# Kernel tuning notes

Hardware: AMD Instinct MI355X
Metric: run time of the kernel (lower is better)

## Reference

```python
import jax, jax.numpy as jnp
import numpy as np


def setup_inputs() -> dict:
    key = jax.random.key(0)
    k1, k2, k3, k4, k5, k6 = jax.random.split(key, 6)
    Ne, dim_in, dim_out, B, Nr, E = 100000, 128, 128, 4, 8, 200000
    return {
        "H": jax.random.normal(k1, (Ne, dim_in), dtype=jnp.float32),
        "A": jax.random.uniform(k2, (Nr, B), dtype=jnp.float32),
        "V": jax.random.uniform(k3, (B, dim_in, dim_out), dtype=jnp.float32),
        "edge_row": jax.random.randint(k4, (Nr, E), 0, Ne, dtype=jnp.int32),
        "edge_col": jax.random.randint(k5, (Nr, E), 0, Ne, dtype=jnp.int32),
        "edge_val": jax.random.uniform(k6, (Nr, E), dtype=jnp.float32),
    }


def reference(H, A, V, edge_row, edge_col, edge_val):
    # W = einsum('rb,bio->rio', A, V): basis-decomposed relation weights
    Ne = H.shape[0]
    Nr = A.shape[0]
    W = jnp.einsum('rb,bio->rio', A, V)            # [Nr, dim_in, dim_out]
    HxW = jnp.einsum('ni,rio->rno', H, W)          # [Nr, Ne, dim_out]
    # sparse T_r @ HxW_r: gather source rows (cols of T), scale by values,
    # scatter-add into destination rows. Done for all relations at once.
    msgs = HxW[jnp.arange(Nr)[:, None], edge_col] * edge_val[..., None]  # [Nr, E, dim_out]
    out = jax.ops.segment_sum(
        msgs.reshape(-1, msgs.shape[-1]),
        edge_row.reshape(-1),
        num_segments=Ne,
    )  # sum over relations folded into one segment_sum
    return out
```

## Files before the change

### kernel.cpp

```cpp
#include <hip/hip_runtime.h>

typedef __attribute__((ext_vector_type(8))) short short8;
typedef __attribute__((ext_vector_type(4))) float floatx4;
typedef __attribute__((ext_vector_type(2))) float floatx2;

constexpr int DIM   = 128;
constexpr int NB    = 4;
constexpr int NR    = 8;
constexpr int BROWS = 512;
constexpr int BCAP  = 16384;

static __device__ __forceinline__ unsigned short f2bf(float f) {
    unsigned int u = __float_as_uint(f);
    u += 0x7FFFu + ((u >> 16) & 1u);
    return (unsigned short)(u >> 16);
}
static __device__ __forceinline__ float bf_lo(unsigned int h) {
    return __uint_as_float(h << 16);
}
static __device__ __forceinline__ float bf_hi(unsigned int h) {
    return __uint_as_float(h & 0xFFFF0000u);
}

__global__ __launch_bounds__(256) void build_vfrag(
    const float* __restrict__ V, unsigned short* __restrict__ VfragG)
{
    int idx  = blockIdx.x * 256 + threadIdx.x;
    int lane = idx & 63;
    int ks   = (idx >> 6) & 3;
    int ot   = (idx >> 8) & 7;
    int b    = idx >> 11;

    int o  = ot * 16 + (lane & 15);
    int kb = ks * 32 + (lane >> 4) * 8;

    short8 v;
#pragma unroll
    for (int j = 0; j < 8; ++j)
        v[j] = (short)f2bf(V[((size_t)b * DIM + kb + j) * DIM + o]);
    *reinterpret_cast<short8*>(VfragG + (size_t)idx * 8) = v;
}

__global__ __launch_bounds__(256) void build_wfrag(
    const float* __restrict__ A, const float* __restrict__ V,
    unsigned short* __restrict__ Wfrag)
{
    int idx  = blockIdx.x * 256 + threadIdx.x;
    int lane = idx & 63;
    int ks   = (idx >> 6) & 3;
    int ot   = (idx >> 8) & 7;
    int r    = idx >> 11;

    int o     = ot * 16 + (lane & 15);
    int kbase = ks * 32 + (lane >> 4) * 8;

    float a0 = A[r * NB + 0], a1 = A[r * NB + 1];
    float a2 = A[r * NB + 2], a3 = A[r * NB + 3];

    short8 v;
#pragma unroll
    for (int j = 0; j < 8; ++j) {
        int k = kbase + j;
        float w = a0 * V[(0 * DIM + k) * DIM + o]
                + a1 * V[(1 * DIM + k) * DIM + o]
                + a2 * V[(2 * DIM + k) * DIM + o]
                + a3 * V[(3 * DIM + k) * DIM + o];
        v[j] = (short)f2bf(w);
    }
    *reinterpret_cast<short8*>(Wfrag + (size_t)idx * 8) = v;
}

__global__ __launch_bounds__(256) void h_to_bf(
    const float* __restrict__ H, unsigned short* __restrict__ Hbf, int n8)
{
    int i = blockIdx.x * 256 + threadIdx.x;
    if (i >= n8) return;
    const float4* hp = reinterpret_cast<const float4*>(H) + (size_t)i * 2;
    float4 f0 = hp[0];
    float4 f1 = hp[1];
    short8 v;
    v[0] = (short)f2bf(f0.x); v[1] = (short)f2bf(f0.y);
    v[2] = (short)f2bf(f0.z); v[3] = (short)f2bf(f0.w);
    v[4] = (short)f2bf(f1.x); v[5] = (short)f2bf(f1.y);
    v[6] = (short)f2bf(f1.z); v[7] = (short)f2bf(f1.w);
    *reinterpret_cast<short8*>(Hbf + (size_t)i * 8) = v;
}

__global__ __launch_bounds__(256) void bucket_scatter(
    const int* __restrict__ erow, const int* __restrict__ ecol,
    const float* __restrict__ eval, int* __restrict__ bcnt,
    int2* __restrict__ sorted1, int n, int E, int chunk)
{
    __shared__ int cnt[256];
    __shared__ int base[256];
    int t = threadIdx.x;
    cnt[t] = 0;
    __syncthreads();

    int s = blockIdx.x * chunk;
    int e = s + chunk; if (e > n) e = n;

    for (int i = s + t; i < e; i += 256)
        atomicAdd(&cnt[erow[i] >> 9], 1);
    __syncthreads();

    int c = cnt[t];
    base[t] = (c > 0) ? atomicAdd(&bcnt[t], c) : 0;
    cnt[t] = 0;
    __syncthreads();

    for (int i = s + t; i < e; i += 256) {
        int row = erow[i];
        int bkt = row >> 9;
        int rank = atomicAdd(&cnt[bkt], 1);
        int r = (int)((unsigned)i / (unsigned)E);
        int2 m;
        m.x = ((row & (BROWS - 1)) << 20) | (r << 17) | ecol[i];
        m.y = __float_as_int(eval[i]);
        sorted1[(size_t)bkt * BCAP + base[bkt] + rank] = m;
    }
}

__global__ __launch_bounds__(1024) void bucket_sort(
    const int2* __restrict__ sorted1, const int* __restrict__ bcnt,
    int* __restrict__ rowStart, int2* __restrict__ sorted, int Ne, int nbuc)
{
    __shared__ int hcnt[BROWS];
    __shared__ int hoff[BROWS];
    __shared__ int sd[256];
    int b = blockIdx.x;
    int t = threadIdx.x;

    for (int i = t; i < BROWS; i += 1024) hcnt[i] = 0;

    if (t < 256) sd[t] = (t < nbuc) ? bcnt[t] : 0;
    __syncthreads();
#pragma unroll
    for (int off = 1; off < 256; off <<= 1) {
        int v = (t < 256 && t >= off) ? sd[t - off] : 0;
        __syncthreads();
        if (t < 256) sd[t] += v;
        __syncthreads();
    }
    if (b == 0 && t == nbuc - 1) rowStart[Ne] = sd[t];

    int n  = bcnt[b];
    int bs = sd[b] - n;
    const int2* src = sorted1 + (size_t)b * BCAP;

    for (int i = t; i < n; i += 1024)
        atomicAdd(&hcnt[(unsigned)src[i].x >> 20], 1);
    __syncthreads();

    if (t < BROWS) hoff[t] = hcnt[t];
    __syncthreads();
#pragma unroll
    for (int off = 1; off < BROWS; off <<= 1) {
        int v = (t < BROWS && t >= off) ? hoff[t - off] : 0;
        __syncthreads();
        if (t < BROWS) hoff[t] += v;
        __syncthreads();
    }
    if (t < BROWS) hoff[t] -= hcnt[t];
    __syncthreads();

    int rs = b * BROWS;
    int nr = Ne - rs; if (nr > BROWS) nr = BROWS;
    for (int j = t; j < nr; j += 1024)
        rowStart[rs + j] = bs + hoff[j];

    for (int i = t; i < BROWS; i += 1024) hcnt[i] = 0;
    __syncthreads();

    for (int i = t; i < n; i += 1024) {
        int2 m = src[i];
        int lr = (unsigned)m.x >> 20;
        int pos = bs + hoff[lr] + atomicAdd(&hcnt[lr], 1);
        sorted[pos] = m;
    }
}

#define AGG_LOAD8(kk, vv, hh, base)                                          \
    _Pragma("unroll")                                                        \
    for (int u = 0; u < 8; ++u) {                                            \
        int2 m = sorted[(base) + u];                                         \
        kk[u] = __builtin_amdgcn_readfirstlane(m.x);                         \
        vv[u] = __uint_as_float(__builtin_amdgcn_readfirstlane(m.y));        \
    }                                                                        \
    _Pragma("unroll")                                                        \
    for (int u = 0; u < 8; ++u)                                              \
        hh[u] = reinterpret_cast<const unsigned int*>(                       \
            Hbf + (size_t)(kk[u] & 0x1FFFF) * DIM)[lane];

#define AGG_FMA8(kk, vv, hh)                                                 \
    _Pragma("unroll")                                                        \
    for (int u = 0; u < 8; ++u) {                                            \
        float4 a = Af[((unsigned)kk[u] >> 17) & 7];                          \
        floatx2 h; h[0] = bf_lo(hh[u]); h[1] = bf_hi(hh[u]);                 \
        float s0 = vv[u] * a.x, s1 = vv[u] * a.y;                            \
        float s2 = vv[u] * a.z, s3 = vv[u] * a.w;                            \
        acc[0] += (floatx2){s0, s0} * h;                                     \
        acc[1] += (floatx2){s1, s1} * h;                                     \
        acc[2] += (floatx2){s2, s2} * h;                                     \
        acc[3] += (floatx2){s3, s3} * h;                                     \
    }

__global__ __launch_bounds__(1024, 4) void fused_kernel(
    const unsigned short* __restrict__ Hbf,
    const int*  __restrict__ rowStart,
    const int2* __restrict__ sorted,
    const float* __restrict__ Aw,
    const unsigned short* __restrict__ VfragG,
    float* __restrict__ out, int Ne, int nTiles)
{
    __shared__ short8 ldsV[8192];
    __shared__ unsigned short ldsA[8192];

    int tid  = threadIdx.x;
    int wave = tid >> 6;
    int lane = tid & 63;
    int quad = lane >> 4, l15 = lane & 15;

    for (int i = tid; i < 8192; i += 1024)
        ldsV[i] = reinterpret_cast<const short8*>(VfragG)[i];

    const float4* Af = reinterpret_cast<const float4*>(Aw);

    unsigned short* aw = ldsA + (size_t)wave * 32
                       + (size_t)(lane >> 4) * 512
                       + (size_t)((lane >> 2) & 3) * 8
                       + (size_t)(lane & 3) * 2;

    for (int tile = blockIdx.x; tile < nTiles; tile += gridDim.x) {
        int node = tile * 16 + wave;
        floatx2 acc[4];
#pragma unroll
        for (int b = 0; b < 4; ++b) acc[b] = (floatx2){0.f, 0.f};

        if (node < Ne) {
            int s = __builtin_amdgcn_readfirstlane(rowStart[node]);
            int e = __builtin_amdgcn_readfirstlane(rowStart[node + 1]);
            int i = s;
            if (i + 8 <= e) {
                int kkA[8], kkB[8];
                float vvA[8], vvB[8];
                unsigned int hhA[8], hhB[8];
                AGG_LOAD8(kkA, vvA, hhA, i); i += 8;
                for (;;) {
                    if (i + 8 <= e) {
                        AGG_LOAD8(kkB, vvB, hhB, i); i += 8;
                        AGG_FMA8(kkA, vvA, hhA);
                    } else { AGG_FMA8(kkA, vvA, hhA); break; }
                    if (i + 8 <= e) {
                        AGG_LOAD8(kkA, vvA, hhA, i); i += 8;
                        AGG_FMA8(kkB, vvB, hhB);
                    } else { AGG_FMA8(kkB, vvB, hhB); break; }
                }
            }
            for (; i < e; ++i) {
                int2 m = sorted[i];
                int k = __builtin_amdgcn_readfirstlane(m.x);
                float v = __uint_as_float(__builtin_amdgcn_readfirstlane(m.y));
                unsigned int hu = reinterpret_cast<const unsigned int*>(
                    Hbf + (size_t)(k & 0x1FFFF) * DIM)[lane];
                float4 a = Af[((unsigned)k >> 17) & 7];
                floatx2 h; h[0] = bf_lo(hu); h[1] = bf_hi(hu);
                float s0 = v * a.x, s1 = v * a.y, s2 = v * a.z, s3 = v * a.w;
                acc[0] += (floatx2){s0, s0} * h;
                acc[1] += (floatx2){s1, s1} * h;
                acc[2] += (floatx2){s2, s2} * h;
                acc[3] += (floatx2){s3, s3} * h;
            }
        }
#pragma unroll
        for (int b = 0; b < 4; ++b) {
            unsigned int pk = (unsigned int)f2bf(acc[b][0])
                            | ((unsigned int)f2bf(acc[b][1]) << 16);
            *reinterpret_cast<unsigned int*>(aw + b * 2048) = pk;
        }
        __syncthreads();

        if (wave < 8) {
            int ot = wave;
            const short8* a8 = reinterpret_cast<const short8*>(ldsA);
            floatx4 vacc = (floatx4){0.f, 0.f, 0.f, 0.f};
#pragma unroll
            for (int b = 0; b < 4; ++b)
#pragma unroll
                for (int ks = 0; ks < 4; ++ks)
                    vacc = __builtin_amdgcn_mfma_f32_16x16x32_bf16(
                        ldsV[((b * 8 + ot) * 4 + ks) * 64 + lane],
                        a8[b * 256 + ks * 64 + l15 * 4 + quad],
                        vacc, 0, 0, 0);

            int onode = tile * 16 + l15;
            if (onode < Ne) {
                float4 st;
                st.x = vacc[0]; st.y = vacc[1]; st.z = vacc[2]; st.w = vacc[3];
                *reinterpret_cast<float4*>(
                    out + (size_t)onode * DIM + ot * 16 + quad * 4) = st;
            }
        }
        __syncthreads();
    }
}

__global__ __launch_bounds__(256) void rgcn_main(
    const unsigned short* __restrict__ Hbf,
    const unsigned short* __restrict__ Wfrag,
    const int*   __restrict__ erow,
    const int*   __restrict__ ecol,
    const float* __restrict__ eval,
    float*       __restrict__ out,
    int E, int groups_per_rel, int waves_per_rel)
{
    int wid  = blockIdx.x * 4 + (threadIdx.x >> 6);
    int lane = threadIdx.x & 63;
    int r    = wid & 7;
    int wr   = wid >> 3;
    int quad = lane >> 4;
    int l15  = lane & 15;

    short8 b[8][4];
    {
        const short8* wp = reinterpret_cast<const short8*>(
            Wfrag + (size_t)r * 16384);
#pragma unroll
        for (int ot = 0; ot < 8; ++ot)
#pragma unroll
            for (int ks = 0; ks < 4; ++ks)
                b[ot][ks] = wp[(ot * 4 + ks) * 64 + lane];
    }

    for (int g = wr; g < groups_per_rel; g += waves_per_rel) {
        int ebase = r * E + g * 16;
        int   colv = ecol[ebase + l15];
        int   rowv = erow[ebase + l15];
        float valv = eval[ebase + l15];

        short8 a[4];
        const unsigned short* hp = Hbf + (size_t)colv * DIM + quad * 8;
#pragma unroll
        for (int ks = 0; ks < 4; ++ks)
            a[ks] = *reinterpret_cast<const short8*>(hp + ks * 32);

        floatx4 acc[8];
#pragma unroll
        for (int ot = 0; ot < 8; ++ot) acc[ot] = (floatx4){0.f, 0.f, 0.f, 0.f};
#pragma unroll
        for (int ot = 0; ot < 8; ++ot)
#pragma unroll
            for (int ks = 0; ks < 4; ++ks)
                acc[ot] = __builtin_amdgcn_mfma_f32_16x16x32_bf16(
                    a[ks], b[ot][ks], acc[ot], 0, 0, 0);

        int   row4[4];
        float val4[4];
#pragma unroll
        for (int reg = 0; reg < 4; ++reg) {
            int src  = quad * 4 + reg;
            row4[reg] = __shfl(rowv, src, 64);
            val4[reg] = __shfl(valv, src, 64);
        }
#pragma unroll
        for (int ot = 0; ot < 8; ++ot)
#pragma unroll
            for (int reg = 0; reg < 4; ++reg) {
                float m = acc[ot][reg] * val4[reg];
                atomicAdd(out + (size_t)row4[reg] * DIM + ot * 16 + l15, m);
            }
    }
}

extern "C" void kernel_launch(void* const* d_in, const int* in_sizes, int n_in,
                              void* d_out, int out_size, void* d_ws, size_t ws_size,
                              hipStream_t stream)
{
    const float* H    = (const float*)d_in[0];
    const float* A    = (const float*)d_in[1];
    const float* V    = (const float*)d_in[2];
    const int*   erow = (const int*)d_in[3];
    const int*   ecol = (const int*)d_in[4];
    const float* eval = (const float*)d_in[5];
    float* out = (float*)d_out;

    int Ne    = in_sizes[0] / DIM;
    int NEtot = in_sizes[3];
    int E     = NEtot / NR;

    auto al = [](size_t x) { return (x + 255) & ~(size_t)255; };

    int nbuc = (Ne + BROWS - 1) / BROWS;
    int nTiles = (Ne + 15) / 16;

    size_t offHbf    = 0;
    size_t offVfrag  = offHbf    + al((size_t)Ne * DIM * 2);
    size_t offWfrag  = offVfrag  + al((size_t)8192 * 16);
    size_t offSort1  = offWfrag  + al((size_t)16384 * 16);
    size_t offRow    = offSort1  + al((size_t)nbuc * BCAP * 8);
    size_t offBcnt   = offRow    + al(((size_t)Ne + 2) * 4);
    size_t offSort   = offBcnt   + al((size_t)256 * 4);
    size_t total     = offSort   + al((size_t)NEtot * 8);

    char* ws = (char*)d_ws;
    unsigned short* Hbf    = (unsigned short*)(ws + offHbf);
    unsigned short* VfragG = (unsigned short*)(ws + offVfrag);
    unsigned short* Wfrag  = (unsigned short*)(ws + offWfrag);

    int n8 = Ne * DIM / 8;
    h_to_bf<<<(n8 + 255) / 256, 256, 0, stream>>>(H, Hbf, n8);

    if (ws_size < total) {
        build_wfrag<<<64, 256, 0, stream>>>(A, V, Wfrag);
        hipMemsetAsync(d_out, 0, (size_t)Ne * DIM * sizeof(float), stream);
        int blocks = 4096;
        int waves_per_rel = blocks * 4 / NR;
        int groups_per_rel = E / 16;
        rgcn_main<<<blocks, 256, 0, stream>>>(Hbf, Wfrag, erow, ecol, eval, out,
                                              E, groups_per_rel, waves_per_rel);
        return;
    }

    int2*           sorted1  = (int2*)(ws + offSort1);
    int*            rowStart = (int*)(ws + offRow);
    int*            bcnt     = (int*)(ws + offBcnt);
    int2*           sorted   = (int2*)(ws + offSort);

    build_vfrag<<<32, 256, 0, stream>>>(V, VfragG);

    hipMemsetAsync(bcnt, 0, 256 * 4, stream);
    int sblocks = 1024;
    int chunk   = (NEtot + sblocks - 1) / sblocks;
    bucket_scatter<<<sblocks, 256, 0, stream>>>(erow, ecol, eval, bcnt,
                                                sorted1, NEtot, E, chunk);
    bucket_sort<<<nbuc, 1024, 0, stream>>>(sorted1, bcnt, rowStart,
                                           sorted, Ne, nbuc);

    fused_kernel<<<256, 1024, 0, stream>>>(Hbf, rowStart, sorted, A,
                                           VfragG, out, Ne, nTiles);
}
```

Baseline: 316.7 us.

## Batch tile aggregation before MFMA, read V fragments from global, fuse prep kernels

Merges the H-to-bf16 conversion, the V fragment build and the bucket-count memset into one prep kernel, cutting launch overhead. The fused kernel now gives each block a contiguous range of tiles and aggregates up to 8 tiles into LDS before a single sync. All 16 waves then run the MFMA projection, instead of only 8 waves after every tile. V fragments are read directly from global/L2 rather than staged in LDS, and an XOR swizzle is added to the LDS layout to reduce bank conflicts. This trades more LDS for the aggregates (128KB per block) for fewer barriers and better MFMA wave use. It risks lower occupancy and extra global traffic for V.

```diff
diff --git a/kernel.cpp b/kernel.cpp
--- a/kernel.cpp
+++ b/kernel.cpp
@@ -9,6 +9,7 @@
 constexpr int NR    = 8;
 constexpr int BROWS = 512;
 constexpr int BCAP  = 16384;
+constexpr int BATCH = 8;
 
 static __device__ __forceinline__ unsigned short f2bf(float f) {
     unsigned int u = __float_as_uint(f);
@@ -86,6 +87,43 @@
     *reinterpret_cast<short8*>(Hbf + (size_t)i * 8) = v;
 }
 
+__global__ __launch_bounds__(256) void prep_kernel(
+    const float* __restrict__ H, unsigned short* __restrict__ Hbf, int n8,
+    const float* __restrict__ V, unsigned short* __restrict__ VfragG,
+    int* __restrict__ bcnt, int nHb)
+{
+    int blk = blockIdx.x;
+    int t   = threadIdx.x;
+    if (blk < nHb) {
+        int i = blk * 256 + t;
+        if (i >= n8) return;
+        const float4* hp = reinterpret_cast<const float4*>(H) + (size_t)i * 2;
+        float4 f0 = hp[0];
+        float4 f1 = hp[1];
+        short8 v;
+        v[0] = (short)f2bf(f0.x); v[1] = (short)f2bf(f0.y);
+        v[2] = (short)f2bf(f0.z); v[3] = (short)f2bf(f0.w);
+        v[4] = (short)f2bf(f1.x); v[5] = (short)f2bf(f1.y);
+        v[6] = (short)f2bf(f1.z); v[7] = (short)f2bf(f1.w);
+        *reinterpret_cast<short8*>(Hbf + (size_t)i * 8) = v;
+    } else if (blk < nHb + 32) {
+        int idx  = (blk - nHb) * 256 + t;
+        int lane = idx & 63;
+        int ks   = (idx >> 6) & 3;
+        int ot   = (idx >> 8) & 7;
+        int b    = idx >> 11;
+        int o  = ot * 16 + (lane & 15);
+        int kb = ks * 32 + (lane >> 4) * 8;
+        short8 v;
+#pragma unroll
+        for (int j = 0; j < 8; ++j)
+            v[j] = (short)f2bf(V[((size_t)b * DIM + kb + j) * DIM + o]);
+        *reinterpret_cast<short8*>(VfragG + (size_t)idx * 8) = v;
+    } else {
+        bcnt[t] = 0;
+    }
+}
+
 __global__ __launch_bounds__(256) void bucket_scatter(
     const int* __restrict__ erow, const int* __restrict__ ecol,
     const float* __restrict__ eval, int* __restrict__ bcnt,
@@ -213,92 +251,104 @@
     const unsigned short* __restrict__ VfragG,
     float* __restrict__ out, int Ne, int nTiles)
 {
-    __shared__ short8 ldsV[8192];
-    __shared__ unsigned short ldsA[8192];
+    __shared__ unsigned short ldsA[BATCH * 8192];
 
     int tid  = threadIdx.x;
     int wave = tid >> 6;
     int lane = tid & 63;
     int quad = lane >> 4, l15 = lane & 15;
 
-    for (int i = tid; i < 8192; i += 1024)
-        ldsV[i] = reinterpret_cast<const short8*>(VfragG)[i];
-
-    const float4* Af = reinterpret_cast<const float4*>(Aw);
-
-    unsigned short* aw = ldsA + (size_t)wave * 32
-                       + (size_t)(lane >> 4) * 512
-                       + (size_t)((lane >> 2) & 3) * 8
-                       + (size_t)(lane & 3) * 2;
-
-    for (int tile = blockIdx.x; tile < nTiles; tile += gridDim.x) {
-        int node = tile * 16 + wave;
-        floatx2 acc[4];
-#pragma unroll
-        for (int b = 0; b < 4; ++b) acc[b] = (floatx2){0.f, 0.f};
-
-        if (node < Ne) {
-            int s = __builtin_amdgcn_readfirstlane(rowStart[node]);
-            int e = __builtin_amdgcn_readfirstlane(rowStart[node + 1]);
-            int i = s;
-            if (i + 8 <= e) {
-                int kkA[8], kkB[8];
-                float vvA[8], vvB[8];
-                unsigned int hhA[8], hhB[8];
-                AGG_LOAD8(kkA, vvA, hhA, i); i += 8;
-                for (;;) {
-                    if (i + 8 <= e) {
-                        AGG_LOAD8(kkB, vvB, hhB, i); i += 8;
-                        AGG_FMA8(kkA, vvA, hhA);
-                    } else { AGG_FMA8(kkA, vvA, hhA); break; }
-                    if (i + 8 <= e) {
-                        AGG_LOAD8(kkA, vvA, hhA, i); i += 8;
-                        AGG_FMA8(kkB, vvB, hhB);
-                    } else { AGG_FMA8(kkB, vvB, hhB); break; }
+    const float4*  Af = reinterpret_cast<const float4*>(Aw);
+    const short8*  Vf = reinterpret_cast<const short8*>(VfragG);
+
+    int t0 = (int)(((long long)blockIdx.x       * nTiles) / gridDim.x);
+    int t1 = (int)(((long long)(blockIdx.x + 1) * nTiles) / gridDim.x);
+
+    int q_ = quad, x_ = (lane >> 2) & 3, y_ = lane & 3;
+    int awBase = q_ * 512 + ((wave ^ (q_ & 1)) * 32) + x_ * 8 + y_ * 2;
+
+    for (int base = t0; base < t1; base += BATCH) {
+        int nsub = t1 - base; if (nsub > BATCH) nsub = BATCH;
+
+        for (int sub = 0; sub < nsub; ++sub) {
+            int node = (base + sub) * 16 + wave;
+            floatx2 acc[4];
+#pragma unroll
+            for (int b = 0; b < 4; ++b) acc[b] = (floatx2){0.f, 0.f};
+
+            if (node < Ne) {
+                int s = __builtin_amdgcn_readfirstlane(rowStart[node]);
+                int e = __builtin_amdgcn_readfirstlane(rowStart[node + 1]);
+                int i = s;
+                if (i + 8 <= e) {
+                    int kkA[8], kkB[8];
+                    float vvA[8], vvB[8];
+                    unsigned int hhA[8], hhB[8];
+                    AGG_LOAD8(kkA, vvA, hhA, i); i += 8;
+                    for (;;) {
+                        if (i + 8 <= e) {
+                            AGG_LOAD8(kkB, vvB, hhB, i); i += 8;
+                            AGG_FMA8(kkA, vvA, hhA);
+                        } else { AGG_FMA8(kkA, vvA, hhA); break; }
+                        if (i + 8 <= e) {
+                            AGG_LOAD8(kkA, vvA, hhA, i); i += 8;
+                            AGG_FMA8(kkB, vvB, hhB);
+                        } else { AGG_FMA8(kkB, vvB, hhB); break; }
+                    }
+                }
+                for (; i < e; ++i) {
+                    int2 m = sorted[i];
+                    int k = __builtin_amdgcn_readfirstlane(m.x);
+                    float v = __uint_as_float(
+                        __builtin_amdgcn_readfirstlane(m.y));
+                    unsigned int hu = reinterpret_cast<const unsigned int*>(
+                        Hbf + (size_t)(k & 0x1FFFF) * DIM)[lane];
+                    float4 a = Af[((unsigned)k >> 17) & 7];
+                    floatx2 h; h[0] = bf_lo(hu); h[1] = bf_hi(hu);
+                    float s0 = v * a.x, s1 = v * a.y;
+                    float s2 = v * a.z, s3 = v * a.w;
+                    acc[0] += (floatx2){s0, s0} * h;
+                    acc[1] += (floatx2){s1, s1} * h;
+                    acc[2] += (floatx2){s2, s2} * h;
+                    acc[3] += (floatx2){s3, s3} * h;
                 }
             }
-            for (; i < e; ++i) {
-                int2 m = sorted[i];
-                int k = __builtin_amdgcn_readfirstlane(m.x);
-                float v = __uint_as_float(__builtin_amdgcn_readfirstlane(m.y));
-                unsigned int hu = reinterpret_cast<const unsigned int*>(
-                    Hbf + (size_t)(k & 0x1FFFF) * DIM)[lane];
-                float4 a = Af[((unsigned)k >> 17) & 7];
-                floatx2 h; h[0] = bf_lo(hu); h[1] = bf_hi(hu);
-                float s0 = v * a.x, s1 = v * a.y, s2 = v * a.z, s3 = v * a.w;
-                acc[0] += (floatx2){s0, s0} * h;
-                acc[1] += (floatx2){s1, s1} * h;
-                acc[2] += (floatx2){s2, s2} * h;
-                acc[3] += (floatx2){s3, s3} * h;
+            unsigned short* aw = ldsA + sub * 8192 + awBase;
+#pragma unroll
+            for (int b = 0; b < 4; ++b) {
+                unsigned int pk = (unsigned int)f2bf(acc[b][0])
+                                | ((unsigned int)f2bf(acc[b][1]) << 16);
+                *reinterpret_cast<unsigned int*>(aw + b * 2048) = pk;
             }
         }
-#pragma unroll
-        for (int b = 0; b < 4; ++b) {
-            unsigned int pk = (unsigned int)f2bf(acc[b][0])
-                            | ((unsigned int)f2bf(acc[b][1]) << 16);
-            *reinterpret_cast<unsigned int*>(aw + b * 2048) = pk;
-        }
-        __syncthreads();
-
-        if (wave < 8) {
-            int ot = wave;
-            const short8* a8 = reinterpret_cast<const short8*>(ldsA);
-            floatx4 vacc = (floatx4){0.f, 0.f, 0.f, 0.f};
-#pragma unroll
-            for (int b = 0; b < 4; ++b)
-#pragma unroll
-                for (int ks = 0; ks < 4; ++ks)
-                    vacc = __builtin_amdgcn_mfma_f32_16x16x32_bf16(
-                        ldsV[((b * 8 + ot) * 4 + ks) * 64 + lane],
-                        a8[b * 256 + ks * 64 + l15 * 4 + quad],
-                        vacc, 0, 0, 0);
-
-            int onode = tile * 16 + l15;
-            if (onode < Ne) {
-                float4 st;
-                st.x = vacc[0]; st.y = vacc[1]; st.z = vacc[2]; st.w = vacc[3];
-                *reinterpret_cast<float4*>(
-                    out + (size_t)onode * DIM + ot * 16 + quad * 4) = st;
+        __syncthreads();
+
+#pragma unroll
+        for (int j = 0; j < 4; ++j) {
+            int task = wave * 4 + j;
+            int sub  = task >> 3, ot = task & 7;
+            if (sub < nsub) {
+                const short8* a8 =
+                    reinterpret_cast<const short8*>(ldsA + sub * 8192);
+                floatx4 vacc = (floatx4){0.f, 0.f, 0.f, 0.f};
+#pragma unroll
+                for (int b = 0; b < 4; ++b)
+#pragma unroll
+                    for (int ks = 0; ks < 4; ++ks)
+                        vacc = __builtin_amdgcn_mfma_f32_16x16x32_bf16(
+                            Vf[((b * 8 + ot) * 4 + ks) * 64 + lane],
+                            a8[b * 256 + ks * 64
+                               + (l15 ^ (ks & 1)) * 4 + quad],
+                            vacc, 0, 0, 0);
+
+                int onode = (base + sub) * 16 + l15;
+                if (onode < Ne) {
+                    float4 st;
+                    st.x = vacc[0]; st.y = vacc[1];
+                    st.z = vacc[2]; st.w = vacc[3];
+                    *reinterpret_cast<float4*>(
+                        out + (size_t)onode * DIM + ot * 16 + quad * 4) = st;
+                }
             }
         }
         __syncthreads();
@@ -407,10 +457,11 @@
     unsigned short* VfragG = (unsigned short*)(ws + offVfrag);
     unsigned short* Wfrag  = (unsigned short*)(ws + offWfrag);
 
-    int n8 = Ne * DIM / 8;
-    h_to_bf<<<(n8 + 255) / 256, 256, 0, stream>>>(H, Hbf, n8);
+    int n8  = Ne * DIM / 8;
+    int nHb = (n8 + 255) / 256;
 
     if (ws_size < total) {
+        h_to_bf<<<nHb, 256, 0, stream>>>(H, Hbf, n8);
         build_wfrag<<<64, 256, 0, stream>>>(A, V, Wfrag);
         hipMemsetAsync(d_out, 0, (size_t)Ne * DIM * sizeof(float), stream);
         int blocks = 4096;
@@ -426,9 +477,9 @@
     int*            bcnt     = (int*)(ws + offBcnt);
     int2*           sorted   = (int2*)(ws + offSort);
 
-    build_vfrag<<<32, 256, 0, stream>>>(V, VfragG);
-
-    hipMemsetAsync(bcnt, 0, 256 * 4, stream);
+    prep_kernel<<<nHb + 32 + 1, 256, 0, stream>>>(H, Hbf, n8, V, VfragG,
+                                                  bcnt, nHb);
+
     int sblocks = 1024;
     int chunk   = (NEtot + sblocks - 1) / sblocks;
     bucket_scatter<<<sblocks, 256, 0, stream>>>(erow, ecol, eval, bcnt,
```

New measurement: 373.2 us. 17.8% more time.
